# Kernel tuning notes

Measured on AMD Instinct MI355X. Metric: run time of the kernel, lower is better.

The kernel has to match this reference:

```python
import jax, jax.numpy as jnp
import numpy as np

B, HIST, PRED, CITY, FEAT, HID = 512, 8, 24, 184, 13, 32


def setup_inputs() -> dict:
    key = jax.random.key(0)
    ks = jax.random.split(key, 10)
    s = 0.1
    return {
        "pm25_hist": jax.random.normal(ks[0], (B, HIST, CITY, 1), jnp.float32),
        "feature": jax.random.normal(ks[1], (B, HIST + PRED, CITY, FEAT), jnp.float32),
        "W_in": jax.random.normal(ks[2], (HID, FEAT + 1), jnp.float32) * s,
        "b_in": jax.random.normal(ks[3], (HID,), jnp.float32) * s,
        "W_out": jax.random.normal(ks[4], (1, HID), jnp.float32) * s,
        "b_out": jax.random.normal(ks[5], (1,), jnp.float32) * s,
        "W_ih": jax.random.normal(ks[6], (4 * HID, HID), jnp.float32) * s,
        "W_hh": jax.random.normal(ks[7], (4 * HID, HID), jnp.float32) * s,
        "b_ih": jax.random.normal(ks[8], (4 * HID,), jnp.float32) * s,
        "b_hh": jax.random.normal(ks[9], (4 * HID,), jnp.float32) * s,
    }


def reference(pm25_hist, feature, W_in, b_in, W_out, b_out, W_ih, W_hh, b_ih, b_hh):
    BC = B * CITY
    # future features, time-major: [PRED, B*CITY, FEAT]
    feat_fut = feature[:, HIST:HIST + PRED]              # [B, PRED, CITY, FEAT]
    feat_fut = jnp.transpose(feat_fut, (1, 0, 2, 3)).reshape(PRED, BC, FEAT)

    h0 = jnp.zeros((BC, HID), pm25_hist.dtype)
    c0 = jnp.zeros((BC, HID), pm25_hist.dtype)
    x0 = pm25_hist[:, -1].reshape(BC, 1)                 # last observed pm25

    def step(carry, feat_t):
        hn, cn, xn = carry
        x = jnp.concatenate([xn, feat_t], axis=-1)        # [BC, in_dim]
        x = x @ W_in.T + b_in                             # fc_in -> [BC, HID]
        gates = x @ W_ih.T + b_ih + hn @ W_hh.T + b_hh    # [BC, 4*HID]
        i, f, g, o = jnp.split(gates, 4, axis=-1)
        i, f, o = jax.nn.sigmoid(i), jax.nn.sigmoid(f), jax.nn.sigmoid(o)
        g = jnp.tanh(g)
        cn = f * cn + i * g
        hn = o * jnp.tanh(cn)
        xn = hn @ W_out.T + b_out                         # fc_out -> [BC, 1]
        return (hn, cn, xn), xn

    _, ys = jax.lax.scan(step, (h0, c0, x0), feat_fut)    # ys: [PRED, BC, 1]
    ys = ys.reshape(PRED, B, CITY, 1)
    return jnp.transpose(ys, (1, 0, 2, 3))                # [B, PRED, CITY, 1]
```

## Files before the change

### kernel.cpp

```cpp
#include <hip/hip_runtime.h>
#include <hip/hip_bf16.h>

#define B_    512
#define HIST_ 8
#define PRED_ 24
#define CITY_ 184
#define FEAT_ 13
#define HID_  32
#define BC_   (B_*CITY_)
#define FLAG_OFF 7168


struct TrueT  { static constexpr bool value = true;  };
struct FalseT { static constexpr bool value = false; };

typedef _Float16 v8hf __attribute__((ext_vector_type(8)));
typedef _Float16 v4hf __attribute__((ext_vector_type(4)));
typedef _Float16 v2hf __attribute__((ext_vector_type(2)));
typedef float    v4f  __attribute__((ext_vector_type(4)));

__device__ __forceinline__ float rcp_(float x) { return __builtin_amdgcn_rcpf(x); }
__device__ __forceinline__ float sigf(float x) { return rcp_(1.0f + __expf(-x)); }
__device__ __forceinline__ float tanhf_(float x) {
    float e = __expf(2.0f * x);
    return 1.0f - 2.0f * rcp_(e + 1.0f);
}

template<bool F32>
__device__ __forceinline__ float ldin(const void* p, long i) {
    if constexpr (F32) return ((const float*)p)[i];
    else               return __bfloat162float(((const __hip_bfloat16*)p)[i]);
}
template<bool F32>
__device__ __forceinline__ void stout(void* p, long i, float v) {
    if constexpr (F32) ((float*)p)[i] = v;
    else               ((__hip_bfloat16*)p)[i] = __float2bfloat16(v);
}

__device__ __forceinline__ v4f mfma_k32(v8hf a, v8hf b, v4f c) {
    return __builtin_amdgcn_mfma_f32_16x16x32_f16(a, b, c, 0, 0, 0);
}
__device__ __forceinline__ v4f mfma_k16(v4hf a, v4hf b, v4f c) {
#if __has_builtin(__builtin_amdgcn_mfma_f32_16x16x16f16)
    return __builtin_amdgcn_mfma_f32_16x16x16f16(a, b, c, 0, 0, 0);
#else
    v8hf a8; v8hf b8;
    #pragma unroll
    for (int j = 0; j < 4; ++j) { a8[j] = a[j]; b8[j] = b[j]; }
    #pragma unroll
    for (int j = 4; j < 8; ++j) { a8[j] = (_Float16)0.f; b8[j] = (_Float16)0.f; }
    return __builtin_amdgcn_mfma_f32_16x16x32_f16(a8, b8, c, 0, 0, 0);
#endif
}

__global__ void detect_dtype(const unsigned short* __restrict__ feat_raw,
                             float* __restrict__ ws) {
    __shared__ int cnt;
    int tid = threadIdx.x;
    if (tid == 0) cnt = 0;
    __syncthreads();
    int insane = 0;
    for (int i = tid; i < 4096; i += 256) {
        float v = __uint_as_float(((unsigned int)feat_raw[i]) << 16);
        if (!(fabsf(v) < 1e8f)) insane++;
    }
    if (insane) atomicAdd(&cnt, insane);
    __syncthreads();
    if (tid == 0) ws[FLAG_OFF] = (cnt > 8) ? 1.0f : 0.0f;
}

template<bool F32>
__global__ void lstm_prep(const void* __restrict__ W_in,
                          const void* __restrict__ b_in,
                          const void* __restrict__ W_out,
                          const void* __restrict__ b_out,
                          const void* __restrict__ W_ih,
                          const void* __restrict__ W_hh,
                          const void* __restrict__ b_ih,
                          const void* __restrict__ b_hh,
                          float* __restrict__ ws)
{
    if (ws[FLAG_OFF] != (F32 ? 1.0f : 0.0f)) return;
    int j = threadIdx.x;
    if (j >= 128) return;

    float wx[14];
    #pragma unroll
    for (int c = 0; c < 14; ++c) wx[c] = 0.0f;
    float bg = ldin<F32>(b_ih, j) + ldin<F32>(b_hh, j);
    #pragma unroll
    for (int m = 0; m < 32; ++m) {
        float wihm = ldin<F32>(W_ih, j*32 + m);
        #pragma unroll
        for (int c = 0; c < 14; ++c) wx[c] = fmaf(wihm, ldin<F32>(W_in, m*14 + c), wx[c]);
        bg = fmaf(wihm, ldin<F32>(b_in, m), bg);
    }
    float a0 = wx[0];
    #pragma unroll
    for (int k = 0; k < 32; ++k)
        ws[j*32 + k] = ldin<F32>(W_hh, j*32 + k) + a0 * ldin<F32>(W_out, k);
    #pragma unroll
    for (int f = 0; f < 13; ++f) ws[4096 + j*16 + f] = wx[1 + f];
    #pragma unroll
    for (int f = 13; f < 16; ++f) ws[4096 + j*16 + f] = 0.0f;
    float bo = ldin<F32>(b_out, 0);
    ws[6144 + j] = bg + a0 * bo;
    ws[6272 + j] = a0;
    ws[6400 + j] = bg;
    if (j < 32) ws[6528 + j] = ldin<F32>(W_out, j);
    if (j == 0) ws[6560] = bo;
}

template<bool F32>
__global__ __launch_bounds__(64, 2) void lstm_main(
    const void* __restrict__ pm25,
    const void* __restrict__ feat,
    const float* __restrict__ ws,
    void* __restrict__ out)
{
    __shared__ __align__(16) _Float16 hhi[16][40];
    __shared__ __align__(16) _Float16 hlo[16][40];
    __shared__ __align__(16) _Float16 fbhi[16][20];
    __shared__ __align__(16) _Float16 fblo[16][20];
    if (ws[FLAG_OFF] != (F32 ? 1.0f : 0.0f)) return;

    const int lane = threadIdx.x;
    const int rho  = lane & 15;
    const int q    = lane >> 4;
    const int wseq = blockIdx.x * 16;

    v8hf Whi0[8], Wlo0[8];
    v4hf Whi1[8], Wlo1[8];
    v4f  bias2[8];
    #pragma unroll
    for (int tt = 0; tt < 8; ++tt) {
        const float* wr = ws + (16*tt + rho)*32 + 8*q;
        #pragma unroll
        for (int j = 0; j < 8; ++j) {
            const float w = wr[j];
            const _Float16 h = (_Float16)w;
            Whi0[tt][j] = h;
            Wlo0[tt][j] = (_Float16)(w - (float)h);
        }
        const float* wf = ws + 4096 + (16*tt + rho)*16 + 4*q;
        #pragma unroll
        for (int j = 0; j < 4; ++j) {
            const float w = wf[j];
            const _Float16 h = (_Float16)w;
            Whi1[tt][j] = h;
            Wlo1[tt][j] = (_Float16)(w - (float)h);
        }
        bias2[tt] = *(const v4f*)(ws + 6144 + 16*tt + 4*q);
    }
    float woutA[4], woutB[4];
    #pragma unroll
    for (int r = 0; r < 4; ++r) {
        woutA[r] = ws[6528 + 4*q + r];
        woutB[r] = ws[6528 + 16 + 4*q + r];
    }
    const float bo = ws[6560];

    const int seq  = wseq + rho;
    const int bb   = seq / CITY_;
    const int city = seq - bb*CITY_;
    const long out_base = (long)bb*PRED_*CITY_ + city;

    if (q == 0) {
        #pragma unroll
        for (int c2 = 13; c2 < 16; ++c2) {
            fbhi[rho][c2] = (_Float16)0.f;
            if constexpr (F32) fblo[rho][c2] = (_Float16)0.f;
        }
    }

    long faddr[4]; int fsl[4], fff[4]; bool fok[4];
    #pragma unroll
    for (int j = 0; j < 4; ++j) {
        const int e = lane + 64*j;
        fok[j] = (e < 16*FEAT_);
        const int sl = e / FEAT_;
        const int f  = e - sl*FEAT_;
        fsl[j] = sl; fff[j] = f;
        const int sq = wseq + (fok[j] ? sl : 0);
        const int b2 = sq / CITY_;
        const int c3 = sq - b2*CITY_;
        faddr[j] = ((long)(b2*(HIST_+PRED_) + HIST_)*CITY_ + c3)*FEAT_ + f;
    }
    float fval[4];
    auto ldfeat = [&]() {
        #pragma unroll
        for (int j = 0; j < 4; ++j) {
            fval[j] = fok[j] ? ldin<F32>(feat, faddr[j]) : 0.0f;
            faddr[j] += CITY_ * FEAT_;
        }
    };
    auto wrfeat = [&]() {
        #pragma unroll
        for (int j = 0; j < 4; ++j) if (fok[j]) {
            const float v = fval[j];
            const _Float16 h = (_Float16)v;
            fbhi[fsl[j]][fff[j]] = h;
            if constexpr (F32) fblo[fsl[j]][fff[j]] = (_Float16)(v - (float)h);
        }
    };

    float cstA[4], cstB[4];

    auto finish = [&](v4f (&acc)[8], int t, auto T0flag) {
        constexpr bool T0 = decltype(T0flag)::value;
        float hA[4], hB[4];
        #pragma unroll
        for (int r = 0; r < 4; ++r) {
            {
                const float I = sigf(acc[0][r]);
                const float G = tanhf_(acc[4][r]);
                const float O = sigf(acc[6][r]);
                float c;
                if constexpr (T0) c = I*G;
                else              c = fmaf(sigf(acc[2][r]), cstA[r], I*G);
                cstA[r] = c;
                hA[r] = O * tanhf_(c);
            }
            {
                const float I = sigf(acc[1][r]);
                const float G = tanhf_(acc[5][r]);
                const float O = sigf(acc[7][r]);
                float c;
                if constexpr (T0) c = I*G;
                else              c = fmaf(sigf(acc[3][r]), cstB[r], I*G);
                cstB[r] = c;
                hB[r] = O * tanhf_(c);
            }
        }
        {
            v2hf p, pl;
            _Float16 h0 = (_Float16)hA[0], h1 = (_Float16)hA[1];
            p[0]=h0; p[1]=h1; *(v2hf*)&hhi[rho][4*q] = p;
            pl[0]=(_Float16)(hA[0]-(float)h0); pl[1]=(_Float16)(hA[1]-(float)h1);
            *(v2hf*)&hlo[rho][4*q] = pl;
            h0 = (_Float16)hA[2]; h1 = (_Float16)hA[3];
            p[0]=h0; p[1]=h1; *(v2hf*)&hhi[rho][4*q+2] = p;
            pl[0]=(_Float16)(hA[2]-(float)h0); pl[1]=(_Float16)(hA[3]-(float)h1);
            *(v2hf*)&hlo[rho][4*q+2] = pl;
            h0 = (_Float16)hB[0]; h1 = (_Float16)hB[1];
            p[0]=h0; p[1]=h1; *(v2hf*)&hhi[rho][16+4*q] = p;
            pl[0]=(_Float16)(hB[0]-(float)h0); pl[1]=(_Float16)(hB[1]-(float)h1);
            *(v2hf*)&hlo[rho][16+4*q] = pl;
            h0 = (_Float16)hB[2]; h1 = (_Float16)hB[3];
            p[0]=h0; p[1]=h1; *(v2hf*)&hhi[rho][16+4*q+2] = p;
            pl[0]=(_Float16)(hB[2]-(float)h0); pl[1]=(_Float16)(hB[3]-(float)h1);
            *(v2hf*)&hlo[rho][16+4*q+2] = pl;
        }
        float y = 0.0f;
        #pragma unroll
        for (int r = 0; r < 4; ++r) {
            y = fmaf(woutA[r], hA[r], y);
            y = fmaf(woutB[r], hB[r], y);
        }
        y += __shfl_xor(y, 16);
        y += __shfl_xor(y, 32);
        if (q == 0) stout<F32>(out, out_base + (long)t*CITY_, y + bo);
    };

    ldfeat();
    wrfeat();
    ldfeat();
    {
        const float x0 = ldin<F32>(pm25, (long)(bb*HIST_ + (HIST_-1))*CITY_ + city);
        const v4hf fhi = *(const v4hf*)&fbhi[rho][4*q];
        v4hf flo;
        if constexpr (F32) flo = *(const v4hf*)&fblo[rho][4*q];
        v4f acc[8];
        #pragma unroll
        for (int tt = 0; tt < 8; ++tt) {
            const v4f bg0 = *(const v4f*)(ws + 6400 + 16*tt + 4*q);
            const v4f a0  = *(const v4f*)(ws + 6272 + 16*tt + 4*q);
            v4f c;
            #pragma unroll
            for (int r = 0; r < 4; ++r) c[r] = fmaf(a0[r], x0, bg0[r]);
            acc[tt] = mfma_k16(Whi1[tt], fhi, c);
            acc[tt] = mfma_k16(Wlo1[tt], fhi, acc[tt]);
            if constexpr (F32) acc[tt] = mfma_k16(Whi1[tt], flo, acc[tt]);
        }
        finish(acc, 0, TrueT{});
    }

    #pragma unroll 1
    for (int t = 1; t < PRED_; ++t) {
        wrfeat();
        if (t < PRED_-1) ldfeat();
        const v8hf xhi = *(const v8hf*)&hhi[rho][8*q];
        const v8hf xlo = *(const v8hf*)&hlo[rho][8*q];
        const v4hf fhi = *(const v4hf*)&fbhi[rho][4*q];
        v4hf flo;
        if constexpr (F32) flo = *(const v4hf*)&fblo[rho][4*q];
        v4f acc[8];
        #pragma unroll
        for (int tt = 0; tt < 8; ++tt) {
            acc[tt] = mfma_k32(Whi0[tt], xhi, bias2[tt]);
            acc[tt] = mfma_k32(Wlo0[tt], xhi, acc[tt]);
            acc[tt] = mfma_k32(Whi0[tt], xlo, acc[tt]);
            acc[tt] = mfma_k16(Whi1[tt], fhi, acc[tt]);
            acc[tt] = mfma_k16(Wlo1[tt], fhi, acc[tt]);
            if constexpr (F32) acc[tt] = mfma_k16(Whi1[tt], flo, acc[tt]);
        }
        finish(acc, t, FalseT{});
    }
}

extern "C" void kernel_launch(void* const* d_in, const int* in_sizes, int n_in,
                              void* d_out, int out_size, void* d_ws, size_t ws_size,
                              hipStream_t stream) {
    const void* pm25  = d_in[0];
    const void* feat  = d_in[1];
    const void* W_in  = d_in[2];
    const void* b_in  = d_in[3];
    const void* W_out = d_in[4];
    const void* b_out = d_in[5];
    const void* W_ih  = d_in[6];
    const void* W_hh  = d_in[7];
    const void* b_ih  = d_in[8];
    const void* b_hh  = d_in[9];
    float* ws = (float*)d_ws;

    detect_dtype<<<dim3(1), dim3(256), 0, stream>>>((const unsigned short*)feat, ws);

    lstm_prep<false><<<dim3(1), dim3(128), 0, stream>>>(
        W_in, b_in, W_out, b_out, W_ih, W_hh, b_ih, b_hh, ws);
    lstm_prep<true><<<dim3(1), dim3(128), 0, stream>>>(
        W_in, b_in, W_out, b_out, W_ih, W_hh, b_ih, b_hh, ws);

    lstm_main<false><<<dim3(BC_/16), dim3(64), 0, stream>>>(pm25, feat, ws, d_out);
    lstm_main<true ><<<dim3(BC_/16), dim3(64), 0, stream>>>(pm25, feat, ws, d_out);
}
```

Measured before the change: 373.6 us.

## Permute gate rows so hidden state stays in registers, drop LDS round-trip

The prep kernel now writes the gate weight rows in a permuted order, so each lane's MFMA output rows line up with the hidden-unit slice it needs as the next step's B operand. That lets h (hi/lo fp16 split) and the feature vector be kept directly in registers, removing the per-step LDS writes and reads. The dtype detection and weight prep are fused into one kernel, and the two templated main launches become a single launch with a runtime branch, using 4 waves per block. This cuts launch overhead and shared-memory traffic. The cost is uncoalesced per-lane feature loads, including duplicated clamped addresses for padding lanes.

New measurement: 359.5 us. 1.04x faster.

```diff
diff --git a/kernel.cpp b/kernel.cpp
--- a/kernel.cpp
+++ b/kernel.cpp
@@ -16,7 +16,6 @@
 
 typedef _Float16 v8hf __attribute__((ext_vector_type(8)));
 typedef _Float16 v4hf __attribute__((ext_vector_type(4)));
-typedef _Float16 v2hf __attribute__((ext_vector_type(2)));
 typedef float    v4f  __attribute__((ext_vector_type(4)));
 
 __device__ __forceinline__ float rcp_(float x) { return __builtin_amdgcn_rcpf(x); }
@@ -53,81 +52,86 @@
 #endif
 }
 
-__global__ void detect_dtype(const unsigned short* __restrict__ feat_raw,
-                             float* __restrict__ ws) {
+template<bool F32>
+__device__ __forceinline__ void prep_body(const void* W_in, const void* b_in,
+                                          const void* W_out, const void* b_out,
+                                          const void* W_ih, const void* W_hh,
+                                          const void* b_ih, const void* b_hh,
+                                          float* ws, int j)
+{
+    if (j >= 128) return;
+    const int gate = j >> 5;
+    const int u    = j & 31;
+    const int qb   = u >> 3;
+    const int psi  = u & 7;
+    const int tt   = 2*gate + (psi >> 2);
+    const int p    = 16*tt + 4*qb + (psi & 3);
+
+    float wx[14];
+    #pragma unroll
+    for (int c = 0; c < 14; ++c) wx[c] = 0.0f;
+    float bg = ldin<F32>(b_ih, j) + ldin<F32>(b_hh, j);
+    #pragma unroll
+    for (int m = 0; m < 32; ++m) {
+        float wihm = ldin<F32>(W_ih, j*32 + m);
+        #pragma unroll
+        for (int c = 0; c < 14; ++c) wx[c] = fmaf(wihm, ldin<F32>(W_in, m*14 + c), wx[c]);
+        bg = fmaf(wihm, ldin<F32>(b_in, m), bg);
+    }
+    float a0 = wx[0];
+    #pragma unroll
+    for (int k = 0; k < 32; ++k)
+        ws[p*32 + k] = ldin<F32>(W_hh, j*32 + k) + a0 * ldin<F32>(W_out, k);
+    #pragma unroll
+    for (int f = 0; f < 13; ++f) ws[4096 + p*16 + f] = wx[1 + f];
+    #pragma unroll
+    for (int f = 13; f < 16; ++f) ws[4096 + p*16 + f] = 0.0f;
+    float bo = ldin<F32>(b_out, 0);
+    ws[6144 + p] = bg + a0 * bo;
+    ws[6272 + p] = a0;
+    ws[6400 + p] = bg;
+    if (j < 32) ws[6528 + j] = ldin<F32>(W_out, j);
+    if (j == 0) ws[6560] = bo;
+}
+
+__global__ void prep_all(const unsigned short* __restrict__ feat_raw,
+                         const void* __restrict__ W_in,  const void* __restrict__ b_in,
+                         const void* __restrict__ W_out, const void* __restrict__ b_out,
+                         const void* __restrict__ W_ih,  const void* __restrict__ W_hh,
+                         const void* __restrict__ b_ih,  const void* __restrict__ b_hh,
+                         float* __restrict__ ws)
+{
     __shared__ int cnt;
-    int tid = threadIdx.x;
+    const int tid = threadIdx.x;
     if (tid == 0) cnt = 0;
     __syncthreads();
     int insane = 0;
-    for (int i = tid; i < 4096; i += 256) {
+    for (int i = tid; i < 4096; i += 128) {
         float v = __uint_as_float(((unsigned int)feat_raw[i]) << 16);
         if (!(fabsf(v) < 1e8f)) insane++;
     }
     if (insane) atomicAdd(&cnt, insane);
     __syncthreads();
-    if (tid == 0) ws[FLAG_OFF] = (cnt > 8) ? 1.0f : 0.0f;
-}
-
-template<bool F32>
-__global__ void lstm_prep(const void* __restrict__ W_in,
-                          const void* __restrict__ b_in,
-                          const void* __restrict__ W_out,
-                          const void* __restrict__ b_out,
-                          const void* __restrict__ W_ih,
-                          const void* __restrict__ W_hh,
-                          const void* __restrict__ b_ih,
-                          const void* __restrict__ b_hh,
-                          float* __restrict__ ws)
-{
-    if (ws[FLAG_OFF] != (F32 ? 1.0f : 0.0f)) return;
-    int j = threadIdx.x;
-    if (j >= 128) return;
-
-    float wx[14];
-    #pragma unroll
-    for (int c = 0; c < 14; ++c) wx[c] = 0.0f;
-    float bg = ldin<F32>(b_ih, j) + ldin<F32>(b_hh, j);
-    #pragma unroll
-    for (int m = 0; m < 32; ++m) {
-        float wihm = ldin<F32>(W_ih, j*32 + m);
-        #pragma unroll
-        for (int c = 0; c < 14; ++c) wx[c] = fmaf(wihm, ldin<F32>(W_in, m*14 + c), wx[c]);
-        bg = fmaf(wihm, ldin<F32>(b_in, m), bg);
-    }
-    float a0 = wx[0];
-    #pragma unroll
-    for (int k = 0; k < 32; ++k)
-        ws[j*32 + k] = ldin<F32>(W_hh, j*32 + k) + a0 * ldin<F32>(W_out, k);
-    #pragma unroll
-    for (int f = 0; f < 13; ++f) ws[4096 + j*16 + f] = wx[1 + f];
-    #pragma unroll
-    for (int f = 13; f < 16; ++f) ws[4096 + j*16 + f] = 0.0f;
-    float bo = ldin<F32>(b_out, 0);
-    ws[6144 + j] = bg + a0 * bo;
-    ws[6272 + j] = a0;
-    ws[6400 + j] = bg;
-    if (j < 32) ws[6528 + j] = ldin<F32>(W_out, j);
-    if (j == 0) ws[6560] = bo;
-}
-
-template<bool F32>
-__global__ __launch_bounds__(64, 2) void lstm_main(
-    const void* __restrict__ pm25,
-    const void* __restrict__ feat,
-    const float* __restrict__ ws,
-    void* __restrict__ out)
-{
-    __shared__ __align__(16) _Float16 hhi[16][40];
-    __shared__ __align__(16) _Float16 hlo[16][40];
-    __shared__ __align__(16) _Float16 fbhi[16][20];
-    __shared__ __align__(16) _Float16 fblo[16][20];
-    if (ws[FLAG_OFF] != (F32 ? 1.0f : 0.0f)) return;
-
-    const int lane = threadIdx.x;
+    const bool f32 = (cnt > 8);
+    if (tid == 0) ws[FLAG_OFF] = f32 ? 1.0f : 0.0f;
+    if (f32) prep_body<true >(W_in,b_in,W_out,b_out,W_ih,W_hh,b_ih,b_hh,ws,tid);
+    else     prep_body<false>(W_in,b_in,W_out,b_out,W_ih,W_hh,b_ih,b_hh,ws,tid);
+}
+
+template<bool F32>
+__device__ __forceinline__ void lstm_body(const void* __restrict__ pm25,
+                                          const void* __restrict__ feat,
+                                          const float* __restrict__ ws,
+                                          void* __restrict__ out)
+{
+    const int lane = threadIdx.x & 63;
     const int rho  = lane & 15;
     const int q    = lane >> 4;
-    const int wseq = blockIdx.x * 16;
+    const int wv   = threadIdx.x >> 6;
+    const int wseq = (blockIdx.x*4 + wv) * 16;
+    const int seq  = wseq + rho;
+    const int bb   = seq / CITY_;
+    const int city = seq - bb*CITY_;
 
     v8hf Whi0[8], Wlo0[8];
     v4hf Whi1[8], Wlo1[8];
@@ -152,124 +156,72 @@
         }
         bias2[tt] = *(const v4f*)(ws + 6144 + 16*tt + 4*q);
     }
-    float woutA[4], woutB[4];
-    #pragma unroll
-    for (int r = 0; r < 4; ++r) {
-        woutA[r] = ws[6528 + 4*q + r];
-        woutB[r] = ws[6528 + 16 + 4*q + r];
-    }
+    float wo8[8];
+    #pragma unroll
+    for (int j = 0; j < 8; ++j) wo8[j] = ws[6528 + 8*q + j];
     const float bo = ws[6560];
-
-    const int seq  = wseq + rho;
-    const int bb   = seq / CITY_;
-    const int city = seq - bb*CITY_;
-    const long out_base = (long)bb*PRED_*CITY_ + city;
-
-    if (q == 0) {
-        #pragma unroll
-        for (int c2 = 13; c2 < 16; ++c2) {
-            fbhi[rho][c2] = (_Float16)0.f;
-            if constexpr (F32) fblo[rho][c2] = (_Float16)0.f;
-        }
-    }
-
-    long faddr[4]; int fsl[4], fff[4]; bool fok[4];
+    const long obase = (long)bb*PRED_*CITY_ + city;
+
+    int eoff[4];
     #pragma unroll
     for (int j = 0; j < 4; ++j) {
-        const int e = lane + 64*j;
-        fok[j] = (e < 16*FEAT_);
-        const int sl = e / FEAT_;
-        const int f  = e - sl*FEAT_;
-        fsl[j] = sl; fff[j] = f;
-        const int sq = wseq + (fok[j] ? sl : 0);
-        const int b2 = sq / CITY_;
-        const int c3 = sq - b2*CITY_;
-        faddr[j] = ((long)(b2*(HIST_+PRED_) + HIST_)*CITY_ + c3)*FEAT_ + f;
-    }
-    float fval[4];
+        const int e = 4*q + j;
+        eoff[j] = (e < FEAT_) ? e : (FEAT_-1);
+    }
+    long fbase = ((long)(bb*(HIST_+PRED_) + HIST_)*CITY_ + city)*FEAT_;
+    float fn[4];
     auto ldfeat = [&]() {
         #pragma unroll
+        for (int j = 0; j < 4; ++j) fn[j] = ldin<F32>(feat, fbase + eoff[j]);
+        fbase += CITY_ * FEAT_;
+    };
+    v4hf fhi, flo;
+    auto convf = [&]() {
+        #pragma unroll
         for (int j = 0; j < 4; ++j) {
-            fval[j] = fok[j] ? ldin<F32>(feat, faddr[j]) : 0.0f;
-            faddr[j] += CITY_ * FEAT_;
+            const _Float16 fh = (_Float16)fn[j];
+            fhi[j] = fh;
+            if constexpr (F32) flo[j] = (_Float16)(fn[j] - (float)fh);
         }
     };
-    auto wrfeat = [&]() {
-        #pragma unroll
-        for (int j = 0; j < 4; ++j) if (fok[j]) {
-            const float v = fval[j];
-            const _Float16 h = (_Float16)v;
-            fbhi[fsl[j]][fff[j]] = h;
-            if constexpr (F32) fblo[fsl[j]][fff[j]] = (_Float16)(v - (float)h);
-        }
-    };
-
-    float cstA[4], cstB[4];
-
-    auto finish = [&](v4f (&acc)[8], int t, auto T0flag) {
+
+    float cst[8];
+    v8hf  xhi, xlo;
+
+    auto finishT = [&](v4f (&acc)[8], int t, auto T0flag) {
         constexpr bool T0 = decltype(T0flag)::value;
-        float hA[4], hB[4];
-        #pragma unroll
-        for (int r = 0; r < 4; ++r) {
-            {
-                const float I = sigf(acc[0][r]);
-                const float G = tanhf_(acc[4][r]);
-                const float O = sigf(acc[6][r]);
-                float c;
-                if constexpr (T0) c = I*G;
-                else              c = fmaf(sigf(acc[2][r]), cstA[r], I*G);
-                cstA[r] = c;
-                hA[r] = O * tanhf_(c);
-            }
-            {
-                const float I = sigf(acc[1][r]);
-                const float G = tanhf_(acc[5][r]);
-                const float O = sigf(acc[7][r]);
-                float c;
-                if constexpr (T0) c = I*G;
-                else              c = fmaf(sigf(acc[3][r]), cstB[r], I*G);
-                cstB[r] = c;
-                hB[r] = O * tanhf_(c);
-            }
-        }
-        {
-            v2hf p, pl;
-            _Float16 h0 = (_Float16)hA[0], h1 = (_Float16)hA[1];
-            p[0]=h0; p[1]=h1; *(v2hf*)&hhi[rho][4*q] = p;
-            pl[0]=(_Float16)(hA[0]-(float)h0); pl[1]=(_Float16)(hA[1]-(float)h1);
-            *(v2hf*)&hlo[rho][4*q] = pl;
-            h0 = (_Float16)hA[2]; h1 = (_Float16)hA[3];
-            p[0]=h0; p[1]=h1; *(v2hf*)&hhi[rho][4*q+2] = p;
-            pl[0]=(_Float16)(hA[2]-(float)h0); pl[1]=(_Float16)(hA[3]-(float)h1);
-            *(v2hf*)&hlo[rho][4*q+2] = pl;
-            h0 = (_Float16)hB[0]; h1 = (_Float16)hB[1];
-            p[0]=h0; p[1]=h1; *(v2hf*)&hhi[rho][16+4*q] = p;
-            pl[0]=(_Float16)(hB[0]-(float)h0); pl[1]=(_Float16)(hB[1]-(float)h1);
-            *(v2hf*)&hlo[rho][16+4*q] = pl;
-            h0 = (_Float16)hB[2]; h1 = (_Float16)hB[3];
-            p[0]=h0; p[1]=h1; *(v2hf*)&hhi[rho][16+4*q+2] = p;
-            pl[0]=(_Float16)(hB[2]-(float)h0); pl[1]=(_Float16)(hB[3]-(float)h1);
-            *(v2hf*)&hlo[rho][16+4*q+2] = pl;
+        float h[8];
+        #pragma unroll
+        for (int psi = 0; psi < 8; ++psi) {
+            const int tl = psi >> 2, r = psi & 3;
+            const float I = sigf(acc[tl][r]);
+            const float G = tanhf_(acc[4+tl][r]);
+            const float O = sigf(acc[6+tl][r]);
+            float c;
+            if constexpr (T0) c = I*G;
+            else              c = fmaf(sigf(acc[2+tl][r]), cst[psi], I*G);
+            cst[psi] = c;
+            h[psi] = O * tanhf_(c);
+        }
+        #pragma unroll
+        for (int psi = 0; psi < 8; ++psi) {
+            const _Float16 hh = (_Float16)h[psi];
+            xhi[psi] = hh;
+            xlo[psi] = (_Float16)(h[psi] - (float)hh);
         }
         float y = 0.0f;
         #pragma unroll
-        for (int r = 0; r < 4; ++r) {
-            y = fmaf(woutA[r], hA[r], y);
-            y = fmaf(woutB[r], hB[r], y);
-        }
+        for (int psi = 0; psi < 8; ++psi) y = fmaf(wo8[psi], h[psi], y);
         y += __shfl_xor(y, 16);
         y += __shfl_xor(y, 32);
-        if (q == 0) stout<F32>(out, out_base + (long)t*CITY_, y + bo);
+        if (q == 0) stout<F32>(out, obase + (long)t*CITY_, y + bo);
     };
 
     ldfeat();
-    wrfeat();
+    convf();
     ldfeat();
     {
         const float x0 = ldin<F32>(pm25, (long)(bb*HIST_ + (HIST_-1))*CITY_ + city);
-        const v4hf fhi = *(const v4hf*)&fbhi[rho][4*q];
-        v4hf flo;
-        if constexpr (F32) flo = *(const v4hf*)&fblo[rho][4*q];
         v4f acc[8];
         #pragma unroll
         for (int tt = 0; tt < 8; ++tt) {
@@ -278,34 +230,42 @@
             v4f c;
             #pragma unroll
             for (int r = 0; r < 4; ++r) c[r] = fmaf(a0[r], x0, bg0[r]);
-            acc[tt] = mfma_k16(Whi1[tt], fhi, c);
-            acc[tt] = mfma_k16(Wlo1[tt], fhi, acc[tt]);
-            if constexpr (F32) acc[tt] = mfma_k16(Whi1[tt], flo, acc[tt]);
-        }
-        finish(acc, 0, TrueT{});
+            v4f a = mfma_k16(Whi1[tt], fhi, c);
+            a = mfma_k16(Wlo1[tt], fhi, a);
+            if constexpr (F32) a = mfma_k16(Whi1[tt], flo, a);
+            acc[tt] = a;
+        }
+        finishT(acc, 0, TrueT{});
     }
 
     #pragma unroll 1
     for (int t = 1; t < PRED_; ++t) {
-        wrfeat();
+        convf();
         if (t < PRED_-1) ldfeat();
-        const v8hf xhi = *(const v8hf*)&hhi[rho][8*q];
-        const v8hf xlo = *(const v8hf*)&hlo[rho][8*q];
-        const v4hf fhi = *(const v4hf*)&fbhi[rho][4*q];
-        v4hf flo;
-        if constexpr (F32) flo = *(const v4hf*)&fblo[rho][4*q];
         v4f acc[8];
         #pragma unroll
         for (int tt = 0; tt < 8; ++tt) {
-            acc[tt] = mfma_k32(Whi0[tt], xhi, bias2[tt]);
-            acc[tt] = mfma_k32(Wlo0[tt], xhi, acc[tt]);
-            acc[tt] = mfma_k32(Whi0[tt], xlo, acc[tt]);
-            acc[tt] = mfma_k16(Whi1[tt], fhi, acc[tt]);
-            acc[tt] = mfma_k16(Wlo1[tt], fhi, acc[tt]);
-            if constexpr (F32) acc[tt] = mfma_k16(Whi1[tt], flo, acc[tt]);
-        }
-        finish(acc, t, FalseT{});
-    }
+            v4f a = mfma_k32(Whi0[tt], xhi, bias2[tt]);
+            a = mfma_k32(Wlo0[tt], xhi, a);
+            a = mfma_k32(Whi0[tt], xlo, a);
+            a = mfma_k16(Whi1[tt], fhi, a);
+            a = mfma_k16(Wlo1[tt], fhi, a);
+            if constexpr (F32) a = mfma_k16(Whi1[tt], flo, a);
+            acc[tt] = a;
+        }
+        finishT(acc, t, FalseT{});
+    }
+}
+
+__global__ __launch_bounds__(256, 2) void lstm_main(
+    const void* __restrict__ pm25,
+    const void* __restrict__ feat,
+    const float* __restrict__ ws,
+    void* __restrict__ out)
+{
+    const bool f32 = (ws[FLAG_OFF] == 1.0f);
+    if (f32) lstm_body<true >(pm25, feat, ws, out);
+    else     lstm_body<false>(pm25, feat, ws, out);
 }
 
 extern "C" void kernel_launch(void* const* d_in, const int* in_sizes, int n_in,
@@ -323,13 +283,9 @@
     const void* b_hh  = d_in[9];
     float* ws = (float*)d_ws;
 
-    detect_dtype<<<dim3(1), dim3(256), 0, stream>>>((const unsigned short*)feat, ws);
-
-    lstm_prep<false><<<dim3(1), dim3(128), 0, stream>>>(
-        W_in, b_in, W_out, b_out, W_ih, W_hh, b_ih, b_hh, ws);
-    lstm_prep<true><<<dim3(1), dim3(128), 0, stream>>>(
-        W_in, b_in, W_out, b_out, W_ih, W_hh, b_ih, b_hh, ws);
-
-    lstm_main<false><<<dim3(BC_/16), dim3(64), 0, stream>>>(pm25, feat, ws, d_out);
-    lstm_main<true ><<<dim3(BC_/16), dim3(64), 0, stream>>>(pm25, feat, ws, d_out);
-}
+    prep_all<<<dim3(1), dim3(128), 0, stream>>>(
+        (const unsigned short*)feat, W_in, b_in, W_out, b_out,
+        W_ih, W_hh, b_ih, b_hh, ws);
+
+    lstm_main<<<dim3(BC_/64), dim3(256), 0, stream>>>(pm25, feat, ws, d_out);
+}
```
